# Optimization experiments

Hardware: AMD Instinct MI355X
Metric: run time of the kernel (lower is better)

The kernel has to match this reference:

```python
import jax, jax.numpy as jnp
import numpy as np
import math

EPS = 1e-5  # torch LayerNorm default


def entmax15(z):
    # Peters & Martins exact sort-based alpha=1.5 entmax along last axis.
    z = z / 2.0
    z = z - jnp.max(z, axis=-1, keepdims=True)
    zs = -jnp.sort(-z, axis=-1)                      # descending
    K = z.shape[-1]
    rho = jnp.arange(1, K + 1, dtype=z.dtype)
    mean = jnp.cumsum(zs, axis=-1) / rho
    mean_sq = jnp.cumsum(zs * zs, axis=-1) / rho
    ss = rho * (mean_sq - mean * mean)
    delta = jnp.clip((1.0 - ss) / rho, 0.0)
    tau = mean - jnp.sqrt(delta)
    k = jnp.sum(tau <= zs, axis=-1, keepdims=True)   # support size
    tau_star = jnp.take_along_axis(tau, k - 1, axis=-1)
    p = jnp.square(jnp.clip(z - tau_star, 0.0))
    return p


def mish(x):
    return x * jnp.tanh(jax.nn.softplus(x))


def layer_norm(x, g, b):
    mu = jnp.mean(x, axis=-1, keepdims=True)
    var = jnp.var(x, axis=-1, keepdims=True)
    return (x - mu) / jnp.sqrt(var + EPS) * g + b


def setup_inputs() -> dict:
    key = jax.random.key(0)
    D, H, F = 512, 8, 2048
    B, S = 8, 1024
    ks = jax.random.split(key, 16)
    s = 1.0 / math.sqrt(D)
    inp = {
        "x": jax.random.normal(ks[0], (B, S, D), jnp.float32),
        # weights stored [in, out]; y = x @ W + b
        "Wq": jax.random.normal(ks[1], (D, D), jnp.float32) * s,
        "bq": jnp.zeros((D,), jnp.float32),
        "Wk": jax.random.normal(ks[2], (D, D), jnp.float32) * s,
        "bk": jnp.zeros((D,), jnp.float32),
        "Wv": jax.random.normal(ks[3], (D, D), jnp.float32) * s,
        "bv": jnp.zeros((D,), jnp.float32),
        "Wo": jax.random.normal(ks[4], (D, D), jnp.float32) * s,
        "bo": jnp.zeros((D,), jnp.float32),
        "g1": jnp.ones((D,), jnp.float32),
        "be1": jnp.zeros((D,), jnp.float32),
        "W1": jax.random.normal(ks[5], (D, F), jnp.float32) * s,
        "b1": jnp.zeros((F,), jnp.float32),
        "W2": jax.random.normal(ks[6], (F, D), jnp.float32) * (1.0 / math.sqrt(F)),
        "b2": jnp.zeros((D,), jnp.float32),
        "g2": jnp.ones((D,), jnp.float32),
        "be2": jnp.zeros((D,), jnp.float32),
    }
    return inp


def reference(x, Wq, bq, Wk, bk, Wv, bv, Wo, bo, g1, be1, W1, b1, W2, b2, g2, be2):
    B, S, D = x.shape
    H = 8
    hd = D // H
    # multi-head self-attention (z = x)
    q = (x @ Wq + bq).reshape(B, S, H, hd).transpose(0, 2, 1, 3)
    k = (x @ Wk + bk).reshape(B, S, H, hd).transpose(0, 2, 1, 3)
    v = (x @ Wv + bv).reshape(B, S, H, hd).transpose(0, 2, 1, 3)
    scores = jnp.einsum("bhqd,bhkd->bhqk", q, k) / math.sqrt(hd)
    attn = entmax15(scores)
    out = jnp.einsum("bhqk,bhkd->bhqd", attn, v)
    out = out.transpose(0, 2, 1, 3).reshape(B, S, D)
    y = out @ Wo + bo
    x = x + layer_norm(y, g1, be1)
    # feed-forward with Mish
    y = mish(x @ W1 + b1) @ W2 + b2
    x = x + layer_norm(y, g2, be2)
    return x
```

## Files before the change

kernel.cpp:

```cpp
#include <hip/hip_runtime.h>


typedef float f32x4 __attribute__((ext_vector_type(4)));
typedef float f32x2 __attribute__((ext_vector_type(2)));
typedef __bf16 b8 __attribute__((ext_vector_type(8)));

#define DEV static __device__ __forceinline__

DEV unsigned short f2bf(float f) {
  return __builtin_bit_cast(unsigned short, (__bf16)f);
}
DEV float bf2f(unsigned short b) { return __uint_as_float(((unsigned)b) << 16); }

DEV float mishf(float x) {
  if (x > 20.f) return x;
  float e = __expf(x);
  float u = 1.f + e;
  u *= u;
  return x * ((u - 1.f) / (u + 1.f));
}

DEV void async16(const void* g, void* l) {
  __builtin_amdgcn_global_load_lds(
      (const __attribute__((address_space(1))) unsigned int*)g,
      (__attribute__((address_space(3))) unsigned int*)l, 16, 0, 0);
}

DEV int mbcnt64(unsigned long long m) {
  return __builtin_amdgcn_mbcnt_hi((unsigned)(m >> 32),
                                   __builtin_amdgcn_mbcnt_lo((unsigned)m, 0));
}

template <int CTRL>
DEV float dppmov(float x) {
  return __builtin_bit_cast(
      float, __builtin_amdgcn_update_dpp(0, __builtin_bit_cast(int, x), CTRL,
                                         0xF, 0xF, true));
}
DEV float swz16(float x) {
  return __builtin_bit_cast(
      float, __builtin_amdgcn_ds_swizzle(__builtin_bit_cast(int, x), 0x401F));
}
DEV float wave_sum(float x) {
  x += dppmov<0xB1>(x);
  x += dppmov<0x4E>(x);
  x += dppmov<0x141>(x);
  x += dppmov<0x140>(x);
  x += swz16(x);
  x += __shfl_xor(x, 32);
  return x;
}
DEV float wave_max(float x) {
  x = fmaxf(x, dppmov<0xB1>(x));
  x = fmaxf(x, dppmov<0x4E>(x));
  x = fmaxf(x, dppmov<0x141>(x));
  x = fmaxf(x, dppmov<0x140>(x));
  x = fmaxf(x, swz16(x));
  x = fmaxf(x, __shfl_xor(x, 32));
  return x;
}

template <int WM, int WN, int EPI, bool OUTBF>
__global__ __launch_bounds__(256) void gemm_bt(
    const unsigned short* __restrict__ A, const unsigned short* __restrict__ Bt,
    const float* __restrict__ bias, void* __restrict__ Cp,
    int K, int lda, int ldb, int ldc,
    long sA1, long sA2, long sB1, long sB2, long sC1, long sC2,
    int hdiv, float alpha) {
  constexpr int BM = WM * 64, BN = WN * 64;
  constexpr int NA = WM * 2, NB = WN * 2;
  __shared__ unsigned short smA[BM * 64];
  __shared__ unsigned short smB[BN * 64];

  const int tid = threadIdx.x;
  const int lane = tid & 63;
  const int z = blockIdx.z;
  const long zi = z / hdiv, zr = z % hdiv;
  const unsigned short* Ab = A + zi * sA1 + zr * sA2 + (long)blockIdx.x * BM * lda;
  const unsigned short* Bb = Bt + zi * sB1 + zr * sB2 + (long)blockIdx.y * BN * ldb;

  int siA[NA];
  const unsigned short* gA[NA];
#pragma unroll
  for (int q = 0; q < NA; ++q) {
    int si = q * 256 + tid;
    int m = si >> 3, s = si & 7, g = s ^ (m & 7);
    siA[q] = si;
    gA[q] = Ab + (long)m * lda + g * 8;
  }
  int siB[NB];
  const unsigned short* gB[NB];
#pragma unroll
  for (int q = 0; q < NB; ++q) {
    int si = q * 256 + tid;
    int m = si >> 3, s = si & 7, g = s ^ (m & 7);
    siB[q] = si;
    gB[q] = Bb + (long)m * ldb + g * 8;
  }

  const int w = tid >> 6;
  const int wr = w / WN, wc = w % WN;
  const int fm = lane & 15, fg = lane >> 4;

  int aOff[4][2], bOff[4][2];
#pragma unroll
  for (int i = 0; i < 4; ++i)
#pragma unroll
    for (int ks = 0; ks < 2; ++ks) {
      int m = wr * 64 + i * 16 + fm;
      aOff[i][ks] = (m * 8 + ((ks * 4 + fg) ^ (fm & 7))) * 8;
      int n = wc * 64 + i * 16 + fm;
      bOff[i][ks] = (n * 8 + ((ks * 4 + fg) ^ (fm & 7))) * 8;
    }

  f32x4 acc[4][4];
#pragma unroll
  for (int i = 0; i < 4; ++i)
#pragma unroll
    for (int j = 0; j < 4; ++j) acc[i][j] = (f32x4){0.f, 0.f, 0.f, 0.f};

  for (int k0 = 0; k0 < K; k0 += 64) {
    __syncthreads();
#pragma unroll
    for (int q = 0; q < NA; ++q) async16(gA[q] + k0, (void*)&smA[siA[q] * 8]);
#pragma unroll
    for (int q = 0; q < NB; ++q) async16(gB[q] + k0, (void*)&smB[siB[q] * 8]);
    __syncthreads();

#pragma unroll
    for (int ks = 0; ks < 2; ++ks) {
      b8 aF[4], bF[4];
#pragma unroll
      for (int i = 0; i < 4; ++i) aF[i] = *(const b8*)&smA[aOff[i][ks]];
#pragma unroll
      for (int j = 0; j < 4; ++j) bF[j] = *(const b8*)&smB[bOff[j][ks]];
#pragma unroll
      for (int i = 0; i < 4; ++i)
#pragma unroll
        for (int j = 0; j < 4; ++j)
          acc[i][j] = __builtin_amdgcn_mfma_f32_16x16x32_bf16(aF[i], bF[j], acc[i][j], 0, 0, 0);
    }
  }

  const long cbase = zi * sC1 + zr * sC2;
  const int row0 = blockIdx.x * BM + wr * 64 + fg * 4;
  const int col0 = blockIdx.y * BN + wc * 64 + fm;
#pragma unroll
  for (int i = 0; i < 4; ++i) {
#pragma unroll
    for (int j = 0; j < 4; ++j) {
      const int col = col0 + j * 16;
      float bv = (EPI >= 1) ? bias[col] : 0.f;
#pragma unroll
      for (int r = 0; r < 4; ++r) {
        const int row = row0 + i * 16 + r;
        float v = acc[i][j][r] * alpha + bv;
        if (EPI == 2) v = mishf(v);
        const long idx = cbase + (long)row * ldc + col;
        if constexpr (OUTBF)
          ((unsigned short*)Cp)[idx] = f2bf(v);
        else
          ((float*)Cp)[idx] = v;
      }
    }
  }
}

__global__ __launch_bounds__(256) void gemm_scores(
    const unsigned short* __restrict__ QKV, unsigned short* __restrict__ P) {
  __shared__ unsigned short smB[128 * 64];

  const int tid = threadIdx.x, lane = tid & 63, w = tid >> 6;
  const int wr = w >> 1, wc = w & 1;
  const int fm = lane & 15, fg = lane >> 4;
  const int z = blockIdx.z, b = z >> 3, h = z & 7;
  const long qrow0 = (long)b * 1024 + blockIdx.x * 128;
  const long krow0 = (long)b * 1024 + blockIdx.y * 128;

#pragma unroll
  for (int q = 0; q < 4; ++q) {
    int si = q * 256 + tid;
    int m = si >> 3, s = si & 7, g = s ^ (m & 7);
    async16(QKV + (krow0 + m) * 1536 + 512 + h * 64 + g * 8, (void*)&smB[si * 8]);
  }

  b8 aQ[4][2];
#pragma unroll
  for (int i = 0; i < 4; ++i) {
    const unsigned short* qp =
        QKV + (qrow0 + wr * 64 + i * 16 + fm) * 1536 + h * 64 + fg * 8;
    aQ[i][0] = *(const b8*)qp;
    aQ[i][1] = *(const b8*)(qp + 32);
  }

  __syncthreads();

  f32x4 acc[4][4];
#pragma unroll
  for (int i = 0; i < 4; ++i)
#pragma unroll
    for (int j = 0; j < 4; ++j) acc[i][j] = (f32x4){0.f, 0.f, 0.f, 0.f};

#pragma unroll
  for (int ks = 0; ks < 2; ++ks) {
    b8 bF[4];
#pragma unroll
    for (int j = 0; j < 4; ++j) {
      int n = wc * 64 + j * 16 + fm;
      bF[j] = *(const b8*)&smB[(n * 8 + ((ks * 4 + fg) ^ (fm & 7))) * 8];
    }
#pragma unroll
    for (int i = 0; i < 4; ++i)
#pragma unroll
      for (int j = 0; j < 4; ++j)
        acc[i][j] = __builtin_amdgcn_mfma_f32_16x16x32_bf16(aQ[i][ks], bF[j], acc[i][j], 0, 0, 0);
  }

  unsigned short* Pb = P + (long)z * 1024 * 1024;
  const int row0 = blockIdx.x * 128 + wr * 64 + fg * 4;
  const int col0 = blockIdx.y * 128 + wc * 64 + fm;
#pragma unroll
  for (int i = 0; i < 4; ++i)
#pragma unroll
    for (int j = 0; j < 4; ++j)
#pragma unroll
      for (int r = 0; r < 4; ++r)
        Pb[(long)(row0 + i * 16 + r) * 1024 + col0 + j * 16] =
            f2bf(acc[i][j][r] * 0.0625f);
}

__global__ __launch_bounds__(256) void gemm_ffn1(
    const unsigned short* __restrict__ A, const unsigned short* __restrict__ Bt,
    const float* __restrict__ bias, unsigned short* __restrict__ C) {
  __shared__ unsigned short smA[2 * 128 * 64];
  __shared__ unsigned short smB[2 * 128 * 64];

  const int tid = threadIdx.x;
  const int lane = tid & 63;
  const unsigned short* Ab = A + (long)blockIdx.x * 128 * 512;
  const unsigned short* Bb = Bt + (long)blockIdx.y * 128 * 512;

  int siA[4], siB[4];
  const unsigned short* gA[4];
  const unsigned short* gB[4];
#pragma unroll
  for (int q = 0; q < 4; ++q) {
    int si = q * 256 + tid;
    int m = si >> 3, s = si & 7, g = s ^ (m & 7);
    siA[q] = si;
    siB[q] = si;
    gA[q] = Ab + (long)m * 512 + g * 8;
    gB[q] = Bb + (long)m * 512 + g * 8;
  }

  const int w = tid >> 6;
  const int wr = w >> 1, wc = w & 1;
  const int fm = lane & 15, fg = lane >> 4;

  int aOff[4][2], bOff[4][2];
#pragma unroll
  for (int i = 0; i < 4; ++i)
#pragma unroll
    for (int ks = 0; ks < 2; ++ks) {
      int m = wr * 64 + i * 16 + fm;
      aOff[i][ks] = (m * 8 + ((ks * 4 + fg) ^ (fm & 7))) * 8;
      int n = wc * 64 + i * 16 + fm;
      bOff[i][ks] = (n * 8 + ((ks * 4 + fg) ^ (fm & 7))) * 8;
    }

  f32x4 acc[4][4];
#pragma unroll
  for (int i = 0; i < 4; ++i)
#pragma unroll
    for (int j = 0; j < 4; ++j) acc[i][j] = (f32x4){0.f, 0.f, 0.f, 0.f};

  auto stage = [&](int buf, int k0) {
    unsigned short* dA = smA + buf * (128 * 64);
    unsigned short* dB = smB + buf * (128 * 64);
#pragma unroll
    for (int q = 0; q < 4; ++q) async16(gA[q] + k0, (void*)&dA[siA[q] * 8]);
#pragma unroll
    for (int q = 0; q < 4; ++q) async16(gB[q] + k0, (void*)&dB[siB[q] * 8]);
  };
  auto compute = [&](int buf) {
    const unsigned short* sA = smA + buf * (128 * 64);
    const unsigned short* sB = smB + buf * (128 * 64);
#pragma unroll
    for (int ks = 0; ks < 2; ++ks) {
      b8 aF[4], bF[4];
#pragma unroll
      for (int i = 0; i < 4; ++i) aF[i] = *(const b8*)&sA[aOff[i][ks]];
#pragma unroll
      for (int j = 0; j < 4; ++j) bF[j] = *(const b8*)&sB[bOff[j][ks]];
#pragma unroll
      for (int i = 0; i < 4; ++i)
#pragma unroll
        for (int j = 0; j < 4; ++j)
          acc[i][j] = __builtin_amdgcn_mfma_f32_16x16x32_bf16(aF[i], bF[j], acc[i][j], 0, 0, 0);
    }
  };

  stage(0, 0);
  __syncthreads();
  int cur = 0;
  for (int k0 = 64; k0 < 512; k0 += 64) {
    stage(cur ^ 1, k0);
    compute(cur);
    __syncthreads();
    cur ^= 1;
  }
  compute(cur);

  const int row0 = blockIdx.x * 128 + wr * 64 + fg * 4;
  const int col0 = blockIdx.y * 128 + wc * 64 + fm;
#pragma unroll
  for (int i = 0; i < 4; ++i) {
#pragma unroll
    for (int j = 0; j < 4; ++j) {
      const int col = col0 + j * 16;
      const float bv = bias[col];
#pragma unroll
      for (int r = 0; r < 4; ++r) {
        const int row = row0 + i * 16 + r;
        C[(long)row * 2048 + col] = f2bf(mishf(acc[i][j][r] + bv));
      }
    }
  }
}

template <int NC>
DEV float solve_tau(const f32x2* zc, float tau) {
  int kprev = -1;
  const f32x2 zero2 = (f32x2){0.f, 0.f};
  for (int it = 0; it < 12; ++it) {
    const f32x2 t2 = (f32x2){tau, tau};
    f32x2 s1v = zero2, s2v = zero2;
    int k = 0;
#pragma unroll
    for (int i = 0; i < NC; ++i) {
      f32x2 h = zc[i] - t2;
      k += __popcll(__ballot(h.x > 0.f));
      k += __popcll(__ballot(h.y > 0.f));
      f32x2 hp = __builtin_elementwise_max(h, zero2);
      s1v += hp;
      s2v += hp * hp;
    }
    float s1 = wave_sum(s1v.x + s1v.y);
    float s2 = wave_sum(s2v.x + s2v.y);
    if (k == kprev) break;
    kprev = k;
    float kf = (float)k;
    float disc = fmaxf(fmaf(s1, s1, -kf * (s2 - 1.f)), 0.f);
    tau += (s1 - __builtin_sqrtf(disc)) / kf;
  }
  return tau;
}

DEV float solve_tau_lds(const float* cw, int nch, int lane, float tau) {
  int kprev = -1;
  const f32x2 zero2 = (f32x2){0.f, 0.f};
  for (int it = 0; it < 12; ++it) {
    const f32x2 t2 = (f32x2){tau, tau};
    f32x2 s1v = zero2, s2v = zero2;
    int k = 0;
    for (int c = 0; c < nch; ++c) {
      f32x2 h = *(const f32x2*)&cw[c * 128 + lane * 2] - t2;
      k += __popcll(__ballot(h.x > 0.f));
      k += __popcll(__ballot(h.y > 0.f));
      f32x2 hp = __builtin_elementwise_max(h, zero2);
      s1v += hp;
      s2v += hp * hp;
    }
    float s1 = wave_sum(s1v.x + s1v.y);
    float s2 = wave_sum(s2v.x + s2v.y);
    if (k == kprev) break;
    kprev = k;
    float kf = (float)k;
    float disc = fmaxf(fmaf(s1, s1, -kf * (s2 - 1.f)), 0.f);
    tau += (s1 - __builtin_sqrtf(disc)) / kf;
  }
  return tau;
}

__global__ __launch_bounds__(256) void entmax_rows(unsigned short* __restrict__ P) {
  const int tid = threadIdx.x, lane = tid & 63, wv = tid >> 6;
  const long row = (long)blockIdx.x * 4 + wv;
  unsigned short* p = P + row * 1024;
  __shared__ float cand[4][1024];

  union { uint4 v; unsigned short u[8]; } a, b;
  a.v = *(const uint4*)(p + lane * 16);
  b.v = *(const uint4*)(p + lane * 16 + 8);
  f32x2 zp[8];
#pragma unroll
  for (int i = 0; i < 4; ++i) {
    zp[i] = (f32x2){bf2f(a.u[2 * i]), bf2f(a.u[2 * i + 1])};
    zp[4 + i] = (f32x2){bf2f(b.u[2 * i]), bf2f(b.u[2 * i + 1])};
  }

  f32x2 mv = zp[0];
#pragma unroll
  for (int i = 1; i < 8; ++i) mv = __builtin_elementwise_max(mv, zp[i]);
  float m = wave_max(fmaxf(mv.x, mv.y));

  const float thr = m - 1.f;
  float* cw = cand[wv];

  int base = 0;
#pragma unroll
  for (int i = 0; i < 8; ++i) {
    unsigned long long mx = __ballot(zp[i].x > thr);
    if (zp[i].x > thr) cw[base + mbcnt64(mx)] = zp[i].x;
    base += __popcll(mx);
    unsigned long long my = __ballot(zp[i].y > thr);
    if (zp[i].y > thr) cw[base + mbcnt64(my)] = zp[i].y;
    base += __popcll(my);
  }

  const int nch = (base + 127) >> 7;
  for (int i = base + lane; i < nch * 128; i += 64) cw[i] = -1e30f;

  float tau;
  if (nch == 1) {
    f32x2 zc[1];
    zc[0] = *(const f32x2*)&cw[lane * 2];
    tau = solve_tau<1>(zc, thr);
  } else if (nch == 2) {
    f32x2 zc[2];
    zc[0] = *(const f32x2*)&cw[lane * 2];
    zc[1] = *(const f32x2*)&cw[128 + lane * 2];
    tau = solve_tau<2>(zc, thr);
  } else {
    tau = solve_tau_lds(cw, nch, lane, thr);
  }

  const f32x2 t2 = (f32x2){tau, tau};
  const f32x2 zero2 = (f32x2){0.f, 0.f};
#pragma unroll
  for (int i = 0; i < 4; ++i) {
    f32x2 h0 = __builtin_elementwise_max(zp[i] - t2, zero2);
    f32x2 h1 = __builtin_elementwise_max(zp[4 + i] - t2, zero2);
    f32x2 p0 = h0 * h0, p1 = h1 * h1;
    a.u[2 * i] = f2bf(p0.x);
    a.u[2 * i + 1] = f2bf(p0.y);
    b.u[2 * i] = f2bf(p1.x);
    b.u[2 * i + 1] = f2bf(p1.y);
  }
  *(uint4*)(p + lane * 16) = a.v;
  *(uint4*)(p + lane * 16 + 8) = b.v;
}

__global__ __launch_bounds__(256) void prep_all(
    const float* __restrict__ x, unsigned short* __restrict__ xb,
    const float* __restrict__ Wq, const float* __restrict__ Wk,
    const float* __restrict__ Wv, const float* __restrict__ Wo,
    const float* __restrict__ W1, const float* __restrict__ W2,
    unsigned short* __restrict__ Wqkvt, unsigned short* __restrict__ Wot,
    unsigned short* __restrict__ W1t, unsigned short* __restrict__ W2t,
    const float* __restrict__ bq, const float* __restrict__ bk,
    const float* __restrict__ bv, float* __restrict__ bqkv) {
  __shared__ float t[32][33];
  const int bid = blockIdx.x, tid = threadIdx.x;

  if (bid < 4096) {
    long i = ((long)bid * 256 + tid) * 4;
    float4 v = *(const float4*)&x[i];
    uint2 pk;
    pk.x = (unsigned)f2bf(v.x) | ((unsigned)f2bf(v.y) << 16);
    pk.y = (unsigned)f2bf(v.z) | ((unsigned)f2bf(v.w) << 16);
    *(uint2*)&xb[i] = pk;
    return;
  }

  const float* in;
  unsigned short* out;
  int ldi, ldo, bx, by;
  if (bid < 5120) {
    int t4 = (bid - 4096) >> 8, local = (bid - 4096) & 255;
    const float* ins[4] = {Wq, Wk, Wv, Wo};
    unsigned short* outs[4] = {Wqkvt, Wqkvt + 512 * 512, Wqkvt + 2 * 512 * 512, Wot};
    in = ins[t4];
    out = outs[t4];
    ldi = 512;
    ldo = 512;
    bx = local & 15;
    by = local >> 4;
  } else if (bid < 6144) {
    int local = bid - 5120;
    in = W1;
    out = W1t;
    ldi = 2048;
    ldo = 512;
    bx = local & 63;
    by = local >> 6;
  } else if (bid < 7168) {
    int local = bid - 6144;
    in = W2;
    out = W2t;
    ldi = 512;
    ldo = 2048;
    bx = local & 15;
    by = local >> 4;
  } else {
    int i = (bid - 7168) * 256 + tid;
    if (i < 512) bqkv[i] = bq[i];
    else if (i < 1024) bqkv[i] = bk[i - 512];
    else if (i < 1536) bqkv[i] = bv[i - 1024];
    return;
  }

  const int tx = tid & 31, ty = tid >> 5;
  const int r0 = by * 32, c0 = bx * 32;
#pragma unroll
  for (int q = 0; q < 4; ++q) {
    int r = ty + q * 8;
    t[r][tx] = in[(long)(r0 + r) * ldi + c0 + tx];
  }
  __syncthreads();
#pragma unroll
  for (int q = 0; q < 4; ++q) {
    int r = ty + q * 8;
    out[(long)(c0 + r) * ldo + r0 + tx] = f2bf(t[tx][r]);
  }
}

__global__ __launch_bounds__(256) void transpose_b2b(const unsigned short* __restrict__ in,
                                                     unsigned short* __restrict__ out,
                                                     int ldi, int ldo, long i1, long i2,
                                                     long o1, long o2, int hdiv) {
  __shared__ unsigned short t[32][33];
  const int z = blockIdx.z;
  in += (long)(z / hdiv) * i1 + (long)(z % hdiv) * i2;
  out += (long)(z / hdiv) * o1 + (long)(z % hdiv) * o2;
  const int tx = threadIdx.x & 31, ty = threadIdx.x >> 5;
  const int r0 = blockIdx.y * 32, c0 = blockIdx.x * 32;
#pragma unroll
  for (int q = 0; q < 4; ++q) {
    int r = ty + q * 8;
    t[r][tx] = in[(long)(r0 + r) * ldi + c0 + tx];
  }
  __syncthreads();
#pragma unroll
  for (int q = 0; q < 4; ++q) {
    int r = ty + q * 8;
    out[(long)(c0 + r) * ldo + r0 + tx] = t[tx][r];
  }
}

template <bool WB, int NS>
__global__ __launch_bounds__(256) void ln_res(const float* __restrict__ xin,
                                              const float* __restrict__ y, long ystr,
                                              const float* __restrict__ ybias,
                                              const float* __restrict__ g,
                                              const float* __restrict__ be,
                                              float* __restrict__ xo,
                                              unsigned short* __restrict__ xob) {
  const int row = blockIdx.x, tid = threadIdx.x, lane = tid & 63, wv = tid >> 6;
  const long base = (long)row * 512 + tid * 2;
  const int c = tid * 2;
  float2 v = *(const float2*)&y[base];
#pragma unroll
  for (int j = 1; j < NS; ++j) {
    float2 u = *(const float2*)&y[base + j * ystr];
    v.x += u.x;
    v.y += u.y;
  }
  v.x += ybias[c];
  v.y += ybias[c + 1];
  float s1 = wave_sum(v.x + v.y);
  float s2 = wave_sum(v.x * v.x + v.y * v.y);
  __shared__ float red[4][2];
  if (lane == 0) {
    red[wv][0] = s1;
    red[wv][1] = s2;
  }
  __syncthreads();
  s1 = red[0][0] + red[1][0] + red[2][0] + red[3][0];
  s2 = red[0][1] + red[1][1] + red[2][1] + red[3][1];
  const float mu = s1 * (1.f / 512.f);
  const float rstd = rsqrtf(s2 * (1.f / 512.f) - mu * mu + 1e-5f);
  float2 xv = *(const float2*)&xin[base];
  float o0 = xv.x + (v.x - mu) * rstd * g[c] + be[c];
  float o1 = xv.y + (v.y - mu) * rstd * g[c + 1] + be[c + 1];
  float2 ov;
  ov.x = o0;
  ov.y = o1;
  *(float2*)&xo[base] = ov;
  if constexpr (WB) {
    unsigned pk = (unsigned)f2bf(o0) | ((unsigned)f2bf(o1) << 16);
    *(unsigned*)&xob[base] = pk;
  }
}

extern "C" void kernel_launch(void* const* d_in, const int* in_sizes, int n_in,
                              void* d_out, int out_size, void* d_ws, size_t ws_size,
                              hipStream_t stream) {
  const int B = 8, S = 1024, D = 512, H = 8, F = 2048;
  const int BS = B * S;
  const int N3 = 3 * D;

  const float* x = (const float*)d_in[0];
  const float* Wq = (const float*)d_in[1];
  const float* bq = (const float*)d_in[2];
  const float* Wk = (const float*)d_in[3];
  const float* bk = (const float*)d_in[4];
  const float* Wv = (const float*)d_in[5];
  const float* bv = (const float*)d_in[6];
  const float* Wo = (const float*)d_in[7];
  const float* bo = (const float*)d_in[8];
  const float* g1 = (const float*)d_in[9];
  const float* be1 = (const float*)d_in[10];
  const float* W1 = (const float*)d_in[11];
  const float* b1 = (const float*)d_in[12];
  const float* W2 = (const float*)d_in[13];
  const float* b2 = (const float*)d_in[14];
  const float* g2 = (const float*)d_in[15];
  const float* be2 = (const float*)d_in[16];
  float* out = (float*)d_out;

  char* w = (char*)d_ws;
  size_t off = 0;
  auto alloc = [&](size_t bytes) -> void* {
    void* p = w + off;
    off += bytes;
    off = (off + 255) & ~(size_t)255;
    return p;
  };

  unsigned short* xb = (unsigned short*)alloc((size_t)BS * D * 2);
  unsigned short* Wqkvt = (unsigned short*)alloc((size_t)N3 * D * 2);
  unsigned short* Wot = (unsigned short*)alloc((size_t)D * D * 2);
  unsigned short* W1t = (unsigned short*)alloc((size_t)F * D * 2);
  unsigned short* W2t = (unsigned short*)alloc((size_t)D * F * 2);
  float* bqkv = (float*)alloc((size_t)N3 * 4);
  unsigned short* QKVb = (unsigned short*)alloc((size_t)BS * N3 * 2);
  unsigned short* Vt = (unsigned short*)alloc((size_t)BS * D * 2);
  unsigned short* attn = (unsigned short*)alloc((size_t)BS * D * 2);
  unsigned short* P = (unsigned short*)alloc((size_t)B * H * S * S * 2);
  float* x1 = (float*)alloc((size_t)BS * D * 4);
  unsigned short* hb = (unsigned short*)alloc((size_t)BS * F * 2);
  unsigned short* x1b = xb;
  float* yp = (float*)P;
  const long PSTR = (long)BS * D;

  const long SS = (long)S * S;
  const long HSS = (long)H * SS;

  prep_all<<<7174, 256, 0, stream>>>(x, xb, Wq, Wk, Wv, Wo, W1, W2,
                                     Wqkvt, Wot, W1t, W2t, bq, bk, bv, bqkv);

  gemm_bt<2, 2, 1, true><<<dim3(BS / 128, N3 / 128, 1), 256, 0, stream>>>(
      xb, Wqkvt, bqkv, QKVb, D, D, D, N3, 0, 0, 0, 0, 0, 0, 1, 1.f);

  transpose_b2b<<<dim3(2, 32, 64), 256, 0, stream>>>(
      QKVb + 1024, Vt, N3, S, (long)S * N3, 64, (long)8 * 64 * S, (long)64 * S, 8);

  gemm_scores<<<dim3(S / 128, S / 128, B * H), 256, 0, stream>>>(QKVb, P);

  entmax_rows<<<(B * H * S) / 4, 256, 0, stream>>>(P);

  gemm_bt<4, 1, 0, true><<<dim3(S / 256, 1, B * H), 256, 0, stream>>>(
      P, Vt, nullptr, attn, S, S, S, D,
      HSS, SS, (long)8 * 64 * S, (long)64 * S, (long)S * D, 64, H, 1.f);

  gemm_bt<2, 2, 0, false><<<dim3(BS / 128, D / 128, 2), 256, 0, stream>>>(
      attn, Wot, nullptr, yp, D / 2, D, D, D, 0, D / 2, 0, D / 2, 0, PSTR, 2, 1.f);

  ln_res<true, 2><<<BS, 256, 0, stream>>>(x, yp, PSTR, bo, g1, be1, x1, x1b);

  gemm_ffn1<<<dim3(BS / 128, F / 128, 1), 256, 0, stream>>>(x1b, W1t, b1, hb);

  gemm_bt<2, 2, 0, false><<<dim3(BS / 128, D / 128, 2), 256, 0, stream>>>(
      hb, W2t, nullptr, yp, F / 2, F, F, D, 0, F / 2, 0, F / 2, 0, PSTR, 2, 1.f);

  ln_res<false, 2><<<BS, 256, 0, stream>>>(x1, yp, PSTR, b2, g2, be2, out, nullptr);
}
```

Before: 336.1 us.

## Fuse entmax probability computation into PV GEMM, store only per-row tau

The entmax kernel now only solves for the per-row threshold tau and writes it to a small buffer instead of rewriting the full score matrix. A new dedicated PV GEMM kernel loads the raw bf16 scores, applies (max(z - tau, 0))^2 on the fly while staging them into LDS, then runs the MFMA against V. This removes one full write pass over the 128 MiB score matrix. The trade-off is that the A operand now goes through synchronous register loads plus conversion instead of async copies, and there is no double buffering, which may stall the MFMA loop.

```diff
diff --git a/kernel.cpp b/kernel.cpp
--- a/kernel.cpp
+++ b/kernel.cpp
@@ -227,6 +227,108 @@
       for (int r = 0; r < 4; ++r)
         Pb[(long)(row0 + i * 16 + r) * 1024 + col0 + j * 16] =
             f2bf(acc[i][j][r] * 0.0625f);
+}
+
+__global__ __launch_bounds__(256) void gemm_pv(
+    const unsigned short* __restrict__ P, const unsigned short* __restrict__ Vt,
+    const float* __restrict__ Tau, unsigned short* __restrict__ attn) {
+  __shared__ unsigned short smA[256 * 64];
+  __shared__ unsigned short smB[64 * 64];
+
+  const int tid = threadIdx.x, lane = tid & 63, w = tid >> 6;
+  const int fm = lane & 15, fg = lane >> 4;
+  const int z = blockIdx.z;
+  const long SS = 1024L * 1024L;
+  const unsigned short* Ab = P + (long)z * SS + (long)blockIdx.x * 256 * 1024;
+  const unsigned short* Bb = Vt + (long)z * 64 * 1024;
+  const float* Tb = Tau + (long)z * 1024 + blockIdx.x * 256;
+
+  int siA[8];
+  const unsigned short* gA[8];
+  float tq[8];
+#pragma unroll
+  for (int q = 0; q < 8; ++q) {
+    int si = q * 256 + tid;
+    int m = si >> 3, s = si & 7, g = s ^ (m & 7);
+    siA[q] = si;
+    gA[q] = Ab + (long)m * 1024 + g * 8;
+    tq[q] = Tb[m];
+  }
+  int siB[2];
+  const unsigned short* gB[2];
+#pragma unroll
+  for (int q = 0; q < 2; ++q) {
+    int si = q * 256 + tid;
+    int m = si >> 3, s = si & 7, g = s ^ (m & 7);
+    siB[q] = si;
+    gB[q] = Bb + (long)m * 1024 + g * 8;
+  }
+
+  int aOff[4][2], bOff[4][2];
+#pragma unroll
+  for (int i = 0; i < 4; ++i)
+#pragma unroll
+    for (int ks = 0; ks < 2; ++ks) {
+      int m = w * 64 + i * 16 + fm;
+      aOff[i][ks] = (m * 8 + ((ks * 4 + fg) ^ (fm & 7))) * 8;
+      int n = i * 16 + fm;
+      bOff[i][ks] = (n * 8 + ((ks * 4 + fg) ^ (fm & 7))) * 8;
+    }
+
+  f32x4 acc[4][4];
+#pragma unroll
+  for (int i = 0; i < 4; ++i)
+#pragma unroll
+    for (int j = 0; j < 4; ++j) acc[i][j] = (f32x4){0.f, 0.f, 0.f, 0.f};
+
+  union AB { b8 v; unsigned short u[8]; };
+  for (int k0 = 0; k0 < 1024; k0 += 64) {
+    __syncthreads();
+    AB areg[8];
+#pragma unroll
+    for (int q = 0; q < 8; ++q) areg[q].v = *(const b8*)(gA[q] + k0);
+#pragma unroll
+    for (int q = 0; q < 2; ++q) async16(gB[q] + k0, (void*)&smB[siB[q] * 8]);
+#pragma unroll
+    for (int q = 0; q < 8; ++q) {
+      AB o;
+#pragma unroll
+      for (int e = 0; e < 8; ++e) {
+        float h = fmaxf(bf2f(areg[q].u[e]) - tq[q], 0.f);
+        o.u[e] = f2bf(h * h);
+      }
+      *(b8*)&smA[siA[q] * 8] = o.v;
+    }
+    __syncthreads();
+
+#pragma unroll
+    for (int ks = 0; ks < 2; ++ks) {
+      b8 aF[4], bF[4];
+#pragma unroll
+      for (int i = 0; i < 4; ++i) aF[i] = *(const b8*)&smA[aOff[i][ks]];
+#pragma unroll
+      for (int j = 0; j < 4; ++j) bF[j] = *(const b8*)&smB[bOff[j][ks]];
+#pragma unroll
+      for (int i = 0; i < 4; ++i)
+#pragma unroll
+        for (int j = 0; j < 4; ++j)
+          acc[i][j] = __builtin_amdgcn_mfma_f32_16x16x32_bf16(aF[i], bF[j], acc[i][j], 0, 0, 0);
+    }
+  }
+
+  const long cbase = (long)(z >> 3) * 1024 * 512 + (z & 7) * 64;
+  const int row0 = blockIdx.x * 256 + w * 64 + fg * 4;
+#pragma unroll
+  for (int i = 0; i < 4; ++i)
+#pragma unroll
+    for (int j = 0; j < 4; ++j) {
+      const int col = fm + j * 16;
+#pragma unroll
+      for (int r = 0; r < 4; ++r) {
+        const int row = row0 + i * 16 + r;
+        attn[cbase + (long)row * 512 + col] = f2bf(acc[i][j][r]);
+      }
+    }
 }
 
 __global__ __launch_bounds__(256) void gemm_ffn1(
@@ -382,10 +484,11 @@
   return tau;
 }
 
-__global__ __launch_bounds__(256) void entmax_rows(unsigned short* __restrict__ P) {
+__global__ __launch_bounds__(256) void entmax_tau(const unsigned short* __restrict__ P,
+                                                  float* __restrict__ T) {
   const int tid = threadIdx.x, lane = tid & 63, wv = tid >> 6;
   const long row = (long)blockIdx.x * 4 + wv;
-  unsigned short* p = P + row * 1024;
+  const unsigned short* p = P + row * 1024;
   __shared__ float cand[4][1024];
 
   union { uint4 v; unsigned short u[8]; } a, b;
@@ -434,20 +537,7 @@
     tau = solve_tau_lds(cw, nch, lane, thr);
   }
 
-  const f32x2 t2 = (f32x2){tau, tau};
-  const f32x2 zero2 = (f32x2){0.f, 0.f};
-#pragma unroll
-  for (int i = 0; i < 4; ++i) {
-    f32x2 h0 = __builtin_elementwise_max(zp[i] - t2, zero2);
-    f32x2 h1 = __builtin_elementwise_max(zp[4 + i] - t2, zero2);
-    f32x2 p0 = h0 * h0, p1 = h1 * h1;
-    a.u[2 * i] = f2bf(p0.x);
-    a.u[2 * i + 1] = f2bf(p0.y);
-    b.u[2 * i] = f2bf(p1.x);
-    b.u[2 * i + 1] = f2bf(p1.y);
-  }
-  *(uint4*)(p + lane * 16) = a.v;
-  *(uint4*)(p + lane * 16 + 8) = b.v;
+  if (lane == 0) T[row] = tau;
 }
 
 __global__ __launch_bounds__(256) void prep_all(
@@ -637,15 +727,13 @@
   unsigned short* Vt = (unsigned short*)alloc((size_t)BS * D * 2);
   unsigned short* attn = (unsigned short*)alloc((size_t)BS * D * 2);
   unsigned short* P = (unsigned short*)alloc((size_t)B * H * S * S * 2);
+  float* Tau = (float*)alloc((size_t)B * H * S * 4);
   float* x1 = (float*)alloc((size_t)BS * D * 4);
   unsigned short* hb = (unsigned short*)alloc((size_t)BS * F * 2);
   unsigned short* x1b = xb;
   float* yp = (float*)P;
   const long PSTR = (long)BS * D;
 
-  const long SS = (long)S * S;
-  const long HSS = (long)H * SS;
-
   prep_all<<<7174, 256, 0, stream>>>(x, xb, Wq, Wk, Wv, Wo, W1, W2,
                                      Wqkvt, Wot, W1t, W2t, bq, bk, bv, bqkv);
 
@@ -657,11 +745,9 @@
 
   gemm_scores<<<dim3(S / 128, S / 128, B * H), 256, 0, stream>>>(QKVb, P);
 
-  entmax_rows<<<(B * H * S) / 4, 256, 0, stream>>>(P);
-
-  gemm_bt<4, 1, 0, true><<<dim3(S / 256, 1, B * H), 256, 0, stream>>>(
-      P, Vt, nullptr, attn, S, S, S, D,
-      HSS, SS, (long)8 * 64 * S, (long)64 * S, (long)S * D, 64, H, 1.f);
+  entmax_tau<<<(B * H * S) / 4, 256, 0, stream>>>(P, Tau);
+
+  gemm_pv<<<dim3(S / 256, 1, B * H), 256, 0, stream>>>(P, Vt, Tau, attn);
 
   gemm_bt<2, 2, 0, false><<<dim3(BS / 128, D / 128, 2), 256, 0, stream>>>(
       attn, Wot, nullptr, yp, D / 2, D, D, D, 0, D / 2, 0, D / 2, 0, PSTR, 2, 1.f);
```

New measurement: 342.4 us. Within noise of the previous version (+1.9%).
